# Performance work log

Measured on AMD Instinct MI355X. Metric: run time of the kernel, lower is better.

## Reference

```python
import jax, jax.numpy as jnp
import numpy as np

N_PTS, N_NODES, N_EDGES, N_CMP = 512, 10000, 50000, 64
# edge types produced by _get_edge_states, plus NULL (do_include_null=True, do_include_all_16=False)
EDGE_TYPES = jnp.array([0, 2, 3, 5, 9], dtype=jnp.int32)  # NULL, NOR, NCONV, NIMPL, AND
N_TYPES = 5
# mapping of temp = 2*a+b in {0,1,2,3} -> edge-type code
TEMP_TO_CODE = jnp.array([2, 3, 5, 9], dtype=jnp.int32)  # NOR, NCONV, NIMPL, AND


def _edge_to_logical(es):
    # es: (n, E) int codes -> (n, N_TYPES*E) bool, type-major layout matching
    # torch.permute([1,0,2]).reshape(n, n_types*n_edges)
    oh = es[:, None, :] == EDGE_TYPES[None, :, None]  # (n, N_TYPES, E)
    return oh.reshape(es.shape[0], N_TYPES * es.shape[1])


def setup_inputs() -> dict:
    key = jax.random.key(0)
    k1, k2, k3 = jax.random.split(key, 3)
    node_activations = jax.random.randint(k1, (N_PTS, N_NODES), 0, 2, dtype=jnp.int32)
    edge_endnode_idx = jax.random.randint(k2, (N_EDGES, 2), 0, N_NODES, dtype=jnp.int32)
    # learned edge states: random categorical over the 5 reachable types
    learned_type_idx = jax.random.randint(k3, (N_CMP, N_EDGES), 0, N_TYPES, dtype=jnp.int32)
    learned_codes = EDGE_TYPES[learned_type_idx]
    binarized_learned = _edge_to_logical(learned_codes).astype(jnp.float32)  # (N_CMP, 5*E)
    return {
        "node_activations": node_activations,
        "binarized_learned": binarized_learned,
        "edge_endnode_idx": edge_endnode_idx,
    }


def reference(node_activations, binarized_learned, edge_endnode_idx):
    # gather endpoint activations: (n_pts, n_edges)
    a = node_activations[:, edge_endnode_idx[:, 0]]
    b = node_activations[:, edge_endnode_idx[:, 1]]
    temp = 2 * a + b  # in {0,1,2,3}
    code = TEMP_TO_CODE[temp]  # edge_type_filter is empty -> no filtering
    # one-hot encode edge states: (n_pts, 5*n_edges)
    bact = _edge_to_logical(code).astype(binarized_learned.dtype)
    # energies: (n_pts, n_cmp); torch does int8 matmul of the same 0/1 values
    energies = jnp.einsum('ck,nk->nc', binarized_learned, bact)
    return energies - jnp.min(energies)
```

## Files before the change

kernel.cpp:

```cpp
#include <hip/hip_runtime.h>
#include <stdint.h>

#define N_PTS   512
#define N_NODES 10000
#define N_EDGES 50000
#define N_CMP   64
#define W64     784
#define EBITS   (W64 * 64)
#define LSTRIDE (N_CMP * W64)
#define NCHUNK  49
#define CW      16
#define TN      16
#define NGRP    (N_PTS / TN)
#define BST_ROW 10016
#define NB_BST  ((N_NODES + 255) / 256)
#define NBLK_L  (NCHUNK * N_CMP)
#define E32SZ   (NGRP * 8 * 64)

typedef unsigned long long u64;

__global__ void build_all(const int* __restrict__ act, const float* __restrict__ BL,
                          u64* __restrict__ Lp, uint16_t* __restrict__ bsT,
                          uint32_t* __restrict__ energy32) {
    int bid = blockIdx.x;
    int t = threadIdx.x;
    if (bid < E32SZ / 256) energy32[bid * 256 + t] = 0;
    if (bid < NBLK_L) {
        __shared__ uint16_t sh[256];
        int c = bid / NCHUNK, bx = bid % NCHUNK;
        int e0 = bx * 1024 + 4 * t;
        int nla = 0, nlb = 0, ntz = 0xF;
        if (e0 < N_EDGES) {
            const float* base = BL + (size_t)c * (5 * N_EDGES) + e0;
            float4 p0 = *(const float4*)(base);
            float4 p2 = *(const float4*)(base + 2 * N_EDGES);
            float4 p3 = *(const float4*)(base + 3 * N_EDGES);
            float4 p4 = *(const float4*)(base + 4 * N_EDGES);
            #define B_(f) ((f) != 0.f ? 1 : 0)
            nla = (B_(p3.x) | B_(p4.x)) | ((B_(p3.y) | B_(p4.y)) << 1)
                | ((B_(p3.z) | B_(p4.z)) << 2) | ((B_(p3.w) | B_(p4.w)) << 3);
            nlb = (B_(p2.x) | B_(p4.x)) | ((B_(p2.y) | B_(p4.y)) << 1)
                | ((B_(p2.z) | B_(p4.z)) << 2) | ((B_(p2.w) | B_(p4.w)) << 3);
            ntz = B_(p0.x) | (B_(p0.y) << 1) | (B_(p0.z) << 2) | (B_(p0.w) << 3);
            #undef B_
        }
        sh[t] = (uint16_t)(nla | (nlb << 4) | (ntz << 8));
        __syncthreads();
        if (t < 48) {
            int p = t >> 4, w = t & 15;
            const u64* v = (const u64*)sh + w * 4;
            u64 word = 0;
            #pragma unroll
            for (int i = 0; i < 4; ++i) {
                u64 x = v[i];
                #pragma unroll
                for (int kk = 0; kk < 4; ++kk)
                    word |= ((x >> (16 * kk + 4 * p)) & 0xFULL) << (4 * (i * 4 + kk));
            }
            Lp[(size_t)p * LSTRIDE + (size_t)c * W64 + bx * 16 + w] = word;
        }
    } else {
        int rem = bid - NBLK_L;
        int g = rem / NB_BST, nb = rem % NB_BST;
        int node = nb * 256 + t;
        if (node < N_NODES) {
            uint32_t m = 0;
            #pragma unroll
            for (int p = 0; p < TN; ++p)
                m |= (act[(size_t)(g * TN + p) * N_NODES + node] != 0 ? 1u : 0u) << p;
            bsT[(size_t)g * BST_ROW + node] = (uint16_t)m;
        }
    }
}

__global__ void __launch_bounds__(512, 6)
match_fused(const u64* __restrict__ Lp, const uint16_t* __restrict__ bsT,
            const int2* __restrict__ edges, uint32_t* __restrict__ energy32) {
    __shared__ u64 Ll[3][CW][65];
    __shared__ __align__(16) uint16_t bsTl[BST_ROW];

    int chunk = blockIdx.x;
    int g = blockIdx.y;
    int t = threadIdx.x;
    int lane = t & 63;
    int wave = t >> 6;
    int cw0 = chunk * CW;

    {
        int w = t & 15;
        #pragma unroll
        for (int pass = 0; pass < 6; ++pass) {
            int r = pass * 32 + (t >> 4);
            int plane = r >> 6, c = r & 63;
            Ll[plane][w][c] = Lp[(size_t)plane * LSTRIDE + (size_t)c * W64 + cw0 + w];
        }
    }
    {
        const uint4* src = (const uint4*)(bsT + (size_t)g * BST_ROW);
        uint4* dst = (uint4*)bsTl;
        for (int idx = t; idx < BST_ROW / 8; idx += 512) dst[idx] = src[idx];
    }
    __syncthreads();

    uint32_t cnt[TN];
    #pragma unroll
    for (int p = 0; p < TN; ++p) cnt[p] = 0;

    #pragma unroll
    for (int j = 0; j < 2; ++j) {
        int w = wave * 2 + j;
        int2 cur = edges[min(chunk * 1024 + w * 64 + lane, N_EDGES - 1)];
        uint32_t a16 = bsTl[cur.x];
        uint32_t b16 = bsTl[cur.y];
        u64 la = Ll[0][w][lane];
        u64 lb = Ll[1][w][lane];
        u64 tz = Ll[2][w][lane];
        #pragma unroll
        for (int p = 0; p < TN; ++p) {
            u64 A = __ballot((a16 >> p) & 1);
            u64 B = __ballot((b16 >> p) & 1);
            cnt[p] += __popcll(tz | (la ^ A) | (lb ^ B));
        }
    }

    __syncthreads();
    uint32_t (*red32)[8][64] = (uint32_t (*)[8][64])bsTl;
    #pragma unroll
    for (int q = 0; q < 8; ++q)
        red32[wave][q][lane] = cnt[2 * q] | (cnt[2 * q + 1] << 16);
    __syncthreads();
    {
        int q = t >> 6, c = t & 63;
        uint32_t s = 0;
        #pragma unroll
        for (int wv = 0; wv < 8; ++wv) s += red32[wv][q][c];
        atomicAdd(&energy32[(g * 8 + q) * 64 + c], s);
    }
}

__global__ void finalize(const uint32_t* __restrict__ energy32, float* __restrict__ out) {
    __shared__ int wm[4];
    __shared__ int ms;
    int t = threadIdx.x;
    int mx = 0;
    const uint4* e4 = (const uint4*)energy32;
    for (int i = t; i < E32SZ / 4; i += 256) {
        uint4 v = e4[i];
        mx = max(mx, (int)(v.x & 0xFFFF)); mx = max(mx, (int)(v.x >> 16));
        mx = max(mx, (int)(v.y & 0xFFFF)); mx = max(mx, (int)(v.y >> 16));
        mx = max(mx, (int)(v.z & 0xFFFF)); mx = max(mx, (int)(v.z >> 16));
        mx = max(mx, (int)(v.w & 0xFFFF)); mx = max(mx, (int)(v.w >> 16));
    }
    for (int off = 32; off; off >>= 1) mx = max(mx, __shfl_down(mx, off, 64));
    if ((t & 63) == 0) wm[t >> 6] = mx;
    __syncthreads();
    if (t == 0) ms = max(max(wm[0], wm[1]), max(wm[2], wm[3]));
    __syncthreads();
    int mxv = ms;
    #pragma unroll
    for (int k = 0; k < 4; ++k) {
        int o = blockIdx.x * 1024 + k * 256 + t;
        int n = o >> 6, c = o & 63;
        int g = n >> 4, p = n & 15, q = p >> 1, h = p & 1;
        uint32_t w = energy32[(g * 8 + q) * 64 + c];
        int s = (int)((w >> (16 * h)) & 0xFFFF);
        out[o] = (float)(mxv - s);
    }
}

extern "C" void kernel_launch(void* const* d_in, const int* in_sizes, int n_in,
                              void* d_out, int out_size, void* d_ws, size_t ws_size,
                              hipStream_t stream) {
    const int*   act   = (const int*)d_in[0];
    const float* BL    = (const float*)d_in[1];
    const int2*  edges = (const int2*)d_in[2];
    float* out = (float*)d_out;

    u64* Lp = (u64*)d_ws;
    uint16_t* bsT = (uint16_t*)(Lp + 3 * (size_t)LSTRIDE);
    uint32_t* energy32 = (uint32_t*)(bsT + (size_t)NGRP * BST_ROW);

    build_all   <<<NBLK_L + NGRP * NB_BST, 256, 0, stream>>>(act, BL, Lp, bsT, energy32);
    match_fused <<<dim3(NCHUNK, NGRP), 512, 0, stream>>>(Lp, bsT, edges, energy32);
    finalize    <<<32, 256, 0, stream>>>(energy32, out);
}
```

Measured before the change: 40.36 us.

## Transpose learned bit-plane layout and read it directly from global memory

The producer kernel now writes the learned bit planes word-major with the component index innermost, so each wave in the match kernel can load its 64 per-lane words contiguously straight from global memory. The shared-memory staging of the learned planes (a strided gather plus its LDS footprint) is removed, and launch bounds are raised to 8 waves per SIMD to allow more occupancy. The cost is that every point-group block rereads the same plane words from L2 instead of staging them once per block, and the producer's stores become strided.

Measured after the change: 39.33 us. 1.03x faster.

```diff
diff --git a/kernel.cpp b/kernel.cpp
--- a/kernel.cpp
+++ b/kernel.cpp
@@ -7,7 +7,6 @@
 #define N_CMP   64
 #define W64     784
 #define EBITS   (W64 * 64)
-#define LSTRIDE (N_CMP * W64)
 #define NCHUNK  49
 #define CW      16
 #define TN      16
@@ -19,8 +18,9 @@
 
 typedef unsigned long long u64;
 
+
 __global__ void build_all(const int* __restrict__ act, const float* __restrict__ BL,
-                          u64* __restrict__ Lp, uint16_t* __restrict__ bsT,
+                          u64* __restrict__ LpT, uint16_t* __restrict__ bsT,
                           uint32_t* __restrict__ energy32) {
     int bid = blockIdx.x;
     int t = threadIdx.x;
@@ -57,7 +57,7 @@
                 for (int kk = 0; kk < 4; ++kk)
                     word |= ((x >> (16 * kk + 4 * p)) & 0xFULL) << (4 * (i * 4 + kk));
             }
-            Lp[(size_t)p * LSTRIDE + (size_t)c * W64 + bx * 16 + w] = word;
+            LpT[((size_t)p * W64 + bx * 16 + w) * 64 + c] = word;
         }
     } else {
         int rem = bid - NBLK_L;
@@ -73,10 +73,9 @@
     }
 }
 
-__global__ void __launch_bounds__(512, 6)
-match_fused(const u64* __restrict__ Lp, const uint16_t* __restrict__ bsT,
+__global__ void __launch_bounds__(512, 8)
+match_fused(const u64* __restrict__ LpT, const uint16_t* __restrict__ bsT,
             const int2* __restrict__ edges, uint32_t* __restrict__ energy32) {
-    __shared__ u64 Ll[3][CW][65];
     __shared__ __align__(16) uint16_t bsTl[BST_ROW];
 
     int chunk = blockIdx.x;
@@ -84,17 +83,7 @@
     int t = threadIdx.x;
     int lane = t & 63;
     int wave = t >> 6;
-    int cw0 = chunk * CW;
 
-    {
-        int w = t & 15;
-        #pragma unroll
-        for (int pass = 0; pass < 6; ++pass) {
-            int r = pass * 32 + (t >> 4);
-            int plane = r >> 6, c = r & 63;
-            Ll[plane][w][c] = Lp[(size_t)plane * LSTRIDE + (size_t)c * W64 + cw0 + w];
-        }
-    }
     {
         const uint4* src = (const uint4*)(bsT + (size_t)g * BST_ROW);
         uint4* dst = (uint4*)bsTl;
@@ -109,12 +98,13 @@
     #pragma unroll
     for (int j = 0; j < 2; ++j) {
         int w = wave * 2 + j;
+        int gw = chunk * CW + w;
         int2 cur = edges[min(chunk * 1024 + w * 64 + lane, N_EDGES - 1)];
+        u64 la = LpT[((size_t)0 * W64 + gw) * 64 + lane];
+        u64 lb = LpT[((size_t)1 * W64 + gw) * 64 + lane];
+        u64 tz = LpT[((size_t)2 * W64 + gw) * 64 + lane];
         uint32_t a16 = bsTl[cur.x];
         uint32_t b16 = bsTl[cur.y];
-        u64 la = Ll[0][w][lane];
-        u64 lb = Ll[1][w][lane];
-        u64 tz = Ll[2][w][lane];
         #pragma unroll
         for (int p = 0; p < TN; ++p) {
             u64 A = __ballot((a16 >> p) & 1);
@@ -176,11 +166,11 @@
     const int2*  edges = (const int2*)d_in[2];
     float* out = (float*)d_out;
 
-    u64* Lp = (u64*)d_ws;
-    uint16_t* bsT = (uint16_t*)(Lp + 3 * (size_t)LSTRIDE);
+    u64* LpT = (u64*)d_ws;
+    uint16_t* bsT = (uint16_t*)(LpT + 3 * (size_t)W64 * 64);
     uint32_t* energy32 = (uint32_t*)(bsT + (size_t)NGRP * BST_ROW);
 
-    build_all   <<<NBLK_L + NGRP * NB_BST, 256, 0, stream>>>(act, BL, Lp, bsT, energy32);
-    match_fused <<<dim3(NCHUNK, NGRP), 512, 0, stream>>>(Lp, bsT, edges, energy32);
+    build_all   <<<NBLK_L + NGRP * NB_BST, 256, 0, stream>>>(act, BL, LpT, bsT, energy32);
+    match_fused <<<dim3(NCHUNK, NGRP), 512, 0, stream>>>(LpT, bsT, edges, energy32);
     finalize    <<<32, 256, 0, stream>>>(energy32, out);
 }
```
